# Kernel optimization log

Measured on AMD Instinct MI355X. Metric: run time of the kernel, lower is better.

Reference implementation:

```python
import jax, jax.numpy as jnp
import numpy as np

B, T, C = 1, 2048, 1024
H = 16
HD = C // H
BLOCK = 2048
NEG = float('-inf')

def setup_inputs() -> dict:
    key = jax.random.key(0)
    ks = jax.random.split(key, 6)
    x = jax.random.normal(ks[0], (B, T, C), dtype=jnp.float32)
    cumulative_scores = jax.random.normal(ks[1], (B, T), dtype=jnp.float32) * 0.1
    padding_mask = jnp.ones((B, T), dtype=jnp.float32)
    token_index = jax.random.randint(ks[2], (B, T), 0, BLOCK).astype(jnp.int64)
    w_attn = jax.random.normal(ks[3], (C, 3 * C), dtype=jnp.float32) * (1.0 / np.sqrt(C))
    b_attn = jnp.zeros((3 * C,), dtype=jnp.float32)
    w_proj = jax.random.normal(ks[4], (C, C), dtype=jnp.float32) * (1.0 / np.sqrt(C))
    b_proj = jnp.zeros((C,), dtype=jnp.float32)
    return dict(x=x, cumulative_scores=cumulative_scores, padding_mask=padding_mask,
                token_index=token_index, w_attn=w_attn, b_attn=b_attn,
                w_proj=w_proj, b_proj=b_proj)

def _rotate_half(z):
    z1, z2 = z[..., : z.shape[-1] // 2], z[..., z.shape[-1] // 2 :]
    return jnp.concatenate((-z2, z1), axis=-1)

def reference(x, cumulative_scores, padding_mask, token_index, w_attn, b_attn, w_proj, b_proj):
    # fused QKV projection
    qkv = x @ w_attn + b_attn                      # (B,T,3C)
    q, k, v = jnp.split(qkv, 3, axis=2)
    q = q.reshape(B, T, H, HD).transpose(0, 2, 1, 3)  # (B,H,T,HD)
    k = k.reshape(B, T, H, HD).transpose(0, 2, 1, 3)
    v = v.reshape(B, T, H, HD).transpose(0, 2, 1, 3)

    # dynamic per-token RoPE positions: global token counts (original scatter
    # broadcasts indices over batch, so counts are global across all batches)
    cnt = jnp.zeros((BLOCK,), jnp.float32).at[token_index.reshape(-1)].add(1.0)
    per_tok = (1.0 / (cnt + 1e-10))[token_index]       # (B,T)
    partial = jnp.cumsum(per_tok, axis=-1)             # (B,T) fractional positions

    inv_freq = 1.0 / (10000.0 ** (jnp.arange(0, HD, 2, dtype=jnp.float32) / HD))
    freqs = partial[..., None] * inv_freq              # (B,T,HD/2)
    emb = jnp.concatenate((freqs, freqs), axis=-1)     # (B,T,HD)
    cos = jnp.cos(emb)[:, None]                        # (B,1,T,HD)
    sin = jnp.sin(emb)[:, None]
    q = q * cos + _rotate_half(q) * sin
    k = k * cos + _rotate_half(k) * sin

    # 'fork' plan: overwrite last channel
    q = q.at[..., -1].set(1.0)
    k = k.at[..., -1].set(jnp.broadcast_to(cumulative_scores[:, None, :], (B, H, T)))

    # additive causal + padding mask (B,T,T)
    causal = jnp.where(jnp.tril(jnp.ones((T, T), jnp.bool_)), 0.0, NEG)
    pm = jnp.take_along_axis(padding_mask, token_index, axis=1)     # (B,T)
    outer = pm[:, :, None] * pm[:, None, :]
    pad_add = jnp.where(outer.astype(jnp.bool_), 0.0, NEG)
    mask = causal[None, :, :] + pad_add                              # (B,T,T)

    # scale v by exp(cumulative_scores)
    v = v * jnp.exp(cumulative_scores)[:, None, :, None]

    scores = jnp.einsum('bhqd,bhkd->bhqk', q, k) / np.sqrt(HD) + mask[:, None]
    probs = jax.nn.softmax(scores, axis=-1)
    y = jnp.einsum('bhqk,bhkd->bhqd', probs, v)        # (B,H,T,HD)
    y = y.transpose(0, 2, 1, 3).reshape(B, T, C)
    return y @ w_proj + b_proj
```

## Files before the change

kernel.cpp:

```cpp
#include <hip/hip_runtime.h>
#include <math.h>

#define T 2048
#define C 1024
#define H 16
#define HD 64
#define N3 (3*C)
#define NBLOCK 2048

typedef __attribute__((ext_vector_type(8))) short bf16x8;
typedef __attribute__((ext_vector_type(4))) float f32x4;

#define MFMA16(a, b, c) __builtin_amdgcn_mfma_f32_16x16x32_bf16((a), (b), (c), 0, 0, 0)

__device__ inline short f2bf(float f) {
    unsigned u; __builtin_memcpy(&u, &f, 4);
    unsigned r = (u + 0x7fffu + ((u >> 16) & 1u)) >> 16;
    return (short)r;
}
__device__ inline float bf2f(short s) {
    unsigned u = ((unsigned)(unsigned short)s) << 16;
    float f; __builtin_memcpy(&f, &u, 4);
    return f;
}

__device__ inline void gload_lds16(const void* g, void* l) {
    __builtin_amdgcn_global_load_lds((const __attribute__((address_space(1))) unsigned int*)g,
                                     (__attribute__((address_space(3))) unsigned int*)l,
                                     16, 0, 0);
}

__global__ __launch_bounds__(256) void pre_kernel(const float* __restrict__ x,
                                                  const float* __restrict__ w_attn,
                                                  const float* __restrict__ w_proj,
                                                  const int* __restrict__ tok,
                                                  const float* __restrict__ padmask,
                                                  short* __restrict__ xb,
                                                  short* __restrict__ wabT,
                                                  short* __restrict__ wpbT,
                                                  float2* __restrict__ tab,
                                                  float* __restrict__ pm_tok) {
    int bid = blockIdx.x;
    int tid = threadIdx.x;
    if (bid == 3072) {
        __shared__ float cntS[NBLOCK];
        __shared__ float sums[256];
        #pragma unroll
        for (int j = 0; j < 8; ++j) cntS[tid * 8 + j] = 0.0f;
        __syncthreads();
        int tk[8];
        #pragma unroll
        for (int j = 0; j < 8; ++j) {
            tk[j] = tok[tid * 8 + j];
            atomicAdd(&cntS[tk[j]], 1.0f);
        }
        __syncthreads();
        float vals[8];
        float s = 0.0f;
        #pragma unroll
        for (int j = 0; j < 8; ++j) {
            s += 1.0f / (cntS[tk[j]] + 1e-10f);
            vals[j] = s;
            pm_tok[tid * 8 + j] = padmask[tk[j]];
        }
        sums[tid] = s;
        __syncthreads();
        for (int off = 1; off < 256; off <<= 1) {
            float v = (tid >= off) ? sums[tid - off] : 0.0f;
            __syncthreads();
            sums[tid] += v;
            __syncthreads();
        }
        float offset = (tid > 0) ? sums[tid - 1] : 0.0f;
        float invf[32];
        #pragma unroll
        for (int j = 0; j < 32; ++j)
            invf[j] = exp2f(-(float)j * (13.287712379549449f / 32.0f));
        #pragma unroll
        for (int e = 0; e < 8; ++e) {
            float p = offset + vals[e];
            float2* row = tab + (tid * 8 + e) * 32;
            #pragma unroll
            for (int j = 0; j < 32; ++j) {
                float s_, c_;
                __sincosf(p * invf[j], &s_, &c_);
                row[j] = make_float2(c_, s_);
            }
        }
        return;
    }
    if (bid < 2048) {
        int i = bid * 1024 + tid * 4;
        float4 v = *(const float4*)(x + i);
        short4 o;
        o.x = f2bf(v.x); o.y = f2bf(v.y); o.z = f2bf(v.z); o.w = f2bf(v.w);
        *(short4*)(xb + i) = o;
        return;
    }
    __shared__ float S[64][65];
    const float* in; short* out; int Kd, Nd, bx, by;
    if (bid < 2816) {
        int b = bid - 2048;
        bx = b % 48; by = b / 48;
        in = w_attn; out = wabT; Kd = C; Nd = N3;
    } else {
        int b = bid - 2816;
        bx = b % 16; by = b / 16;
        in = w_proj; out = wpbT; Kd = C; Nd = C;
    }
    int n0 = bx * 64, k0 = by * 64;
    #pragma unroll
    for (int i = 0; i < 16; ++i) {
        int lin = tid + i * 256;
        int r = lin >> 6, c = lin & 63;
        S[r][c] = in[(size_t)(k0 + r) * Nd + n0 + c];
    }
    __syncthreads();
    #pragma unroll
    for (int i = 0; i < 16; ++i) {
        int lin = tid + i * 256;
        int rn = lin >> 6, ck = lin & 63;
        out[(size_t)(n0 + rn) * Kd + k0 + ck] = f2bf(S[ck][rn]);
    }
}

template <int EPI>
__global__ __launch_bounds__(256) void gemm128x64(const short* __restrict__ A,
                                                  const short* __restrict__ Bt,
                                                  const float* __restrict__ bias,
                                                  void* __restrict__ Cout,
                                                  int N, int K,
                                                  const float2* __restrict__ tab,
                                                  const float* __restrict__ cumsc,
                                                  const float* __restrict__ pm_tok,
                                                  short* __restrict__ vbT) {
    __shared__ alignas(16) short As[2][128 * 64];
    __shared__ alignas(16) short Bs[2][64 * 64];
    int tid = threadIdx.x;
    int m0 = blockIdx.y * 128, n0 = blockIdx.x * 64;
    int w = tid >> 6, l = tid & 63;
    int lq = l & 15, g = l >> 4;
    int urow = l >> 3;
    int sw_col = ((l & 7) ^ urow) * 8;

    f32x4 acc[2][4] = {};

    auto stage = [&](int buf, int k0) {
        #pragma unroll
        for (int i = 0; i < 4; ++i) {
            int u = w * 4 + i;
            gload_lds16(A + (size_t)(m0 + u * 8 + urow) * K + k0 + sw_col, As[buf] + u * 512);
        }
        #pragma unroll
        for (int i = 0; i < 2; ++i) {
            int u = w * 2 + i;
            gload_lds16(Bt + (size_t)(n0 + u * 8 + urow) * K + k0 + sw_col, Bs[buf] + u * 512);
        }
    };

    int NK = K / 64;
    stage(0, 0);
    asm volatile("s_waitcnt vmcnt(0)" ::: "memory");
    __builtin_amdgcn_s_barrier();
    __builtin_amdgcn_sched_barrier(0);

    for (int t = 0; t < NK; ++t) {
        int cur = t & 1;
        if (t + 1 < NK) stage(cur ^ 1, (t + 1) * 64);
        #pragma unroll
        for (int kk = 0; kk < 2; ++kk) {
            bf16x8 af[2], bfr[4];
            #pragma unroll
            for (int fi = 0; fi < 2; ++fi) {
                int rd = w * 32 + fi * 16 + lq;
                af[fi] = *(const bf16x8*)(As[cur] + rd * 64 + (((kk * 4 + g) ^ (rd & 7)) * 8));
            }
            #pragma unroll
            for (int fj = 0; fj < 4; ++fj) {
                int rd = fj * 16 + lq;
                bfr[fj] = *(const bf16x8*)(Bs[cur] + rd * 64 + (((kk * 4 + g) ^ (rd & 7)) * 8));
            }
            __builtin_amdgcn_s_setprio(1);
            #pragma unroll
            for (int fi = 0; fi < 2; ++fi)
                #pragma unroll
                for (int fj = 0; fj < 4; ++fj)
                    acc[fi][fj] = MFMA16(af[fi], bfr[fj], acc[fi][fj]);
            __builtin_amdgcn_s_setprio(0);
        }
        asm volatile("s_waitcnt vmcnt(0)" ::: "memory");
        __builtin_amdgcn_s_barrier();
        __builtin_amdgcn_sched_barrier(0);
    }

    if (EPI == 0) {
        float* Cf = (float*)Cout;
        #pragma unroll
        for (int fi = 0; fi < 2; ++fi)
            #pragma unroll
            for (int r = 0; r < 4; ++r) {
                int m = m0 + w * 32 + fi * 16 + g * 4 + r;
                #pragma unroll
                for (int fj = 0; fj < 4; ++fj) {
                    int n = n0 + fj * 16 + lq;
                    Cf[(size_t)m * N + n] = acc[fi][fj][r] + bias[n];
                }
            }
    } else {
        short* Cb = (short*)Cout;
        int nt = n0 >> 6;
        if (nt < 32) {
            bool isQ = (nt < 16);
            #pragma unroll
            for (int fi = 0; fi < 2; ++fi)
                #pragma unroll
                for (int r = 0; r < 4; ++r) {
                    int trow = m0 + w * 32 + fi * 16 + g * 4 + r;
                    float pm = pm_tok[trow];
                    float csc = cumsc[trow];
                    float2 cs0 = tab[trow * 32 + lq];
                    float2 cs1 = tab[trow * 32 + 16 + lq];
                    float a0 = acc[fi][0][r] + bias[n0 + lq];
                    float a1 = acc[fi][1][r] + bias[n0 + 16 + lq];
                    float a2 = acc[fi][2][r] + bias[n0 + 32 + lq];
                    float a3 = acc[fi][3][r] + bias[n0 + 48 + lq];
                    float lo0 = a0 * cs0.x - a2 * cs0.y;
                    float hi0 = a2 * cs0.x + a0 * cs0.y;
                    float lo1 = a1 * cs1.x - a3 * cs1.y;
                    float hi1 = a3 * cs1.x + a1 * cs1.y;
                    if (lq == 15)
                        hi1 = isQ ? ((pm != 0.0f) ? 1.0f : 0.0f)
                                  : ((pm != 0.0f) ? csc : -1e20f);
                    size_t base = (size_t)trow * N3 + n0;
                    Cb[base + lq]      = f2bf(lo0);
                    Cb[base + 16 + lq] = f2bf(lo1);
                    Cb[base + 32 + lq] = f2bf(hi0);
                    Cb[base + 48 + lq] = f2bf(hi1);
                }
        } else {
            int h = nt - 32;
            short* Sv = &As[0][0];
            __syncthreads();
            #pragma unroll
            for (int fi = 0; fi < 2; ++fi)
                #pragma unroll
                for (int r = 0; r < 4; ++r) {
                    int tloc = w * 32 + fi * 16 + g * 4 + r;
                    float ef = __expf(cumsc[m0 + tloc]);
                    #pragma unroll
                    for (int fj = 0; fj < 4; ++fj) {
                        int d = fj * 16 + lq;
                        Sv[d * 136 + tloc] = f2bf((acc[fi][fj][r] + bias[n0 + d]) * ef);
                    }
                }
            __syncthreads();
            #pragma unroll
            for (int e = 0; e < 4; ++e) {
                int idx = tid * 4 + e;
                int d = idx >> 4, t8 = (idx & 15) * 8;
                bf16x8 o = *(const bf16x8*)(Sv + d * 136 + t8);
                *(bf16x8*)(vbT + (size_t)(h * 64 + d) * T + m0 + t8) = o;
            }
        }
    }
}

__global__ __launch_bounds__(256) void attn_flash(const short* __restrict__ qkvb,
                                                  const short* __restrict__ vbT,
                                                  short* __restrict__ yb) {
    __shared__ alignas(16) short Kt[2][64 * 64];
    __shared__ alignas(16) short Vt[2][64 * 64];
    __shared__ alignas(16) short Ps[4][16][72];

    int b = blockIdx.x;
    int h, qt;
    if (b < 256) { h = b & 15; qt = 31 - (b >> 4); }
    else         { int c2 = b - 256; h = c2 & 15; qt = c2 >> 4; }
    int tid = threadIdx.x;
    int w = tid >> 6, l = tid & 63;
    int lq = l & 15, g = l >> 4;
    int qrl = w * 16 + lq;

    const short* qbase = qkvb + (size_t)(qt * 64 + qrl) * N3 + h * 64;
    bf16x8 qf0 = *(const bf16x8*)(qbase + g * 8);
    bf16x8 qf1 = *(const bf16x8*)(qbase + 32 + g * 8);

    f32x4 accO[4] = {};
    float lsum = 0.0f;

    int srow = tid >> 3, scol = (tid & 7) * 8;
    const short* kgb = qkvb + C + h * 64 + scol;
    const short* vgb = vbT + (size_t)(h * 64) * T + scol;
    int wb0 = srow * 128 + ((scol * 2) ^ ((srow & 7) << 4));
    int wb1 = (srow + 32) * 128 + ((scol * 2) ^ ((srow & 7) << 4));

    auto do_tile = [&](int cur, bool masked) {
        const char* Kc = (const char*)Kt[cur];
        const char* Vc = (const char*)Vt[cur];
        f32x4 s[4] = {};
        __builtin_amdgcn_s_setprio(1);
        #pragma unroll
        for (int f = 0; f < 4; ++f) {
            int row = f * 16 + lq;
            const char* kr_ = Kc + row * 128;
            int sw = (row & 7) << 4;
            bf16x8 a0 = *(const bf16x8*)(kr_ + ((g * 16) ^ sw));
            bf16x8 a1 = *(const bf16x8*)(kr_ + ((64 + g * 16) ^ sw));
            s[f] = MFMA16(a0, qf0, s[f]);
            s[f] = MFMA16(a1, qf1, s[f]);
        }
        __builtin_amdgcn_s_setprio(0);
        float p[16];
        #pragma unroll
        for (int f = 0; f < 4; ++f)
            #pragma unroll
            for (int r = 0; r < 4; ++r) {
                float sv = s[f][r] * 0.125f;
                if (masked) {
                    int kl = f * 16 + g * 4 + r;
                    sv = (kl > qrl) ? -INFINITY : sv;
                }
                float pv = __expf(sv);
                p[f * 4 + r] = pv;
                lsum += pv;
            }
        #pragma unroll
        for (int f = 0; f < 4; ++f) {
            unsigned u0, u1;
            asm("v_cvt_pk_bf16_f32 %0, %1, %2" : "=v"(u0) : "v"(p[f * 4 + 0]), "v"(p[f * 4 + 1]));
            asm("v_cvt_pk_bf16_f32 %0, %1, %2" : "=v"(u1) : "v"(p[f * 4 + 2]), "v"(p[f * 4 + 3]));
            uint2 uu; uu.x = u0; uu.y = u1;
            *(uint2*)&Ps[w][lq][f * 16 + g * 4] = uu;
        }
        __builtin_amdgcn_s_setprio(1);
        #pragma unroll
        for (int kh = 0; kh < 2; ++kh) {
            bf16x8 pa = *(const bf16x8*)&Ps[w][lq][kh * 32 + g * 8];
            #pragma unroll
            for (int f = 0; f < 4; ++f) {
                int vrow = f * 16 + lq;
                const char* vr_ = Vc + vrow * 128;
                bf16x8 vb = *(const bf16x8*)(vr_ + (((kh * 32 + g * 8) * 2) ^ ((vrow & 7) << 4)));
                accO[f] = MFMA16(pa, vb, accO[f]);
            }
        }
        __builtin_amdgcn_s_setprio(0);
    };

    uint4 kr0 = *(const uint4*)(kgb + (size_t)srow * N3);
    uint4 kr1 = *(const uint4*)(kgb + (size_t)(srow + 32) * N3);
    uint4 vr0 = *(const uint4*)(vgb + (size_t)srow * T);
    uint4 vr1 = *(const uint4*)(vgb + (size_t)(srow + 32) * T);
    *(uint4*)((char*)Kt[0] + wb0) = kr0;
    *(uint4*)((char*)Kt[0] + wb1) = kr1;
    *(uint4*)((char*)Vt[0] + wb0) = vr0;
    *(uint4*)((char*)Vt[0] + wb1) = vr1;
    __syncthreads();

    for (int t = 0; t < qt; ++t) {
        int kn = (t + 1) * 64;
        kr0 = *(const uint4*)(kgb + (size_t)(kn + srow) * N3);
        kr1 = *(const uint4*)(kgb + (size_t)(kn + srow + 32) * N3);
        vr0 = *(const uint4*)(vgb + (size_t)srow * T + kn);
        vr1 = *(const uint4*)(vgb + (size_t)(srow + 32) * T + kn);

        do_tile(t & 1, false);

        int nxt = (t & 1) ^ 1;
        *(uint4*)((char*)Kt[nxt] + wb0) = kr0;
        *(uint4*)((char*)Kt[nxt] + wb1) = kr1;
        *(uint4*)((char*)Vt[nxt] + wb0) = vr0;
        *(uint4*)((char*)Vt[nxt] + wb1) = vr1;
        __syncthreads();
    }
    do_tile(qt & 1, true);

    lsum += __shfl_xor(lsum, 16);
    lsum += __shfl_xor(lsum, 32);
    float linv_own = 1.0f / lsum;
    float li[4];
    #pragma unroll
    for (int r = 0; r < 4; ++r) li[r] = __shfl(linv_own, g * 4 + r);

    #pragma unroll
    for (int f = 0; f < 4; ++f)
        #pragma unroll
        for (int r = 0; r < 4; ++r) {
            int trow = qt * 64 + w * 16 + g * 4 + r;
            yb[(size_t)trow * C + h * 64 + f * 16 + lq] = f2bf(accO[f][r] * li[r]);
        }
}

extern "C" void kernel_launch(void* const* d_in, const int* in_sizes, int n_in,
                              void* d_out, int out_size, void* d_ws, size_t ws_size,
                              hipStream_t stream) {
    const float* x       = (const float*)d_in[0];
    const float* cumsc   = (const float*)d_in[1];
    const float* padmask = (const float*)d_in[2];
    const int*   tok     = (const int*)d_in[3];
    const float* w_attn  = (const float*)d_in[4];
    const float* b_attn  = (const float*)d_in[5];
    const float* w_proj  = (const float*)d_in[6];
    const float* b_proj  = (const float*)d_in[7];
    float* out = (float*)d_out;

    float*  pm_tok = (float*)d_ws;
    float2* tab    = (float2*)(pm_tok + 2048);
    short*  xb     = (short*)(pm_tok + 2048 + 131072);
    short*  wabT   = xb + (size_t)T * C;
    short*  wpbT   = wabT + (size_t)N3 * C;
    short*  qkvb   = wpbT + (size_t)C * C;
    short*  vbT    = qkvb + (size_t)T * N3;
    short*  yb     = vbT + (size_t)C * T;

    pre_kernel<<<3073, 256, 0, stream>>>(x, w_attn, w_proj, tok, padmask,
                                         xb, wabT, wpbT, tab, pm_tok);
    gemm128x64<1><<<dim3(48, 16), 256, 0, stream>>>(xb, wabT, b_attn, qkvb, N3, C,
                                                    tab, cumsc, pm_tok, vbT);
    attn_flash<<<512, 256, 0, stream>>>(qkvb, vbT, yb);
    gemm128x64<0><<<dim3(16, 16), 256, 0, stream>>>(yb, wpbT, b_proj, out, C, C,
                                                    nullptr, nullptr, nullptr, nullptr);
}
```

Measured before the change: 94.67 us.

## Retile GEMMs to 128xBN with BK=32 and 2x2 warp grid, direct V-transpose stores

```diff
diff --git a/kernel.cpp b/kernel.cpp
--- a/kernel.cpp
+++ b/kernel.cpp
@@ -124,41 +124,43 @@
     }
 }
 
-template <int EPI>
-__global__ __launch_bounds__(256) void gemm128x64(const short* __restrict__ A,
-                                                  const short* __restrict__ Bt,
-                                                  const float* __restrict__ bias,
-                                                  void* __restrict__ Cout,
-                                                  int N, int K,
-                                                  const float2* __restrict__ tab,
-                                                  const float* __restrict__ cumsc,
-                                                  const float* __restrict__ pm_tok,
-                                                  short* __restrict__ vbT) {
-    __shared__ alignas(16) short As[2][128 * 64];
-    __shared__ alignas(16) short Bs[2][64 * 64];
+template <int OUT_BF16, int BNF, int EPI>
+__global__ __launch_bounds__(256) void gemm_bt(const short* __restrict__ A,
+                                               const short* __restrict__ Bt,
+                                               const float* __restrict__ bias,
+                                               void* __restrict__ Cout,
+                                               int M, int N, int K,
+                                               const float2* __restrict__ tab,
+                                               const float* __restrict__ cumsc,
+                                               const float* __restrict__ pm_tok,
+                                               short* __restrict__ vbT) {
+    constexpr int BN = BNF * 32;
+    __shared__ alignas(16) short As[2][128 * 32];
+    __shared__ alignas(16) short Bs[2][BN * 32];
     int tid = threadIdx.x;
-    int m0 = blockIdx.y * 128, n0 = blockIdx.x * 64;
+    int m0 = blockIdx.y * 128, n0 = blockIdx.x * BN;
     int w = tid >> 6, l = tid & 63;
+    int wm = (w >> 1) * 64, wn = (w & 1) * (BNF * 16);
     int lq = l & 15, g = l >> 4;
-    int urow = l >> 3;
-    int sw_col = ((l & 7) ^ urow) * 8;
-
-    f32x4 acc[2][4] = {};
+    int prow = l >> 2, pcol = (l & 3) * 8;
+    f32x4 acc[4][BNF] = {};
 
     auto stage = [&](int buf, int k0) {
         #pragma unroll
-        for (int i = 0; i < 4; ++i) {
-            int u = w * 4 + i;
-            gload_lds16(A + (size_t)(m0 + u * 8 + urow) * K + k0 + sw_col, As[buf] + u * 512);
-        }
-        #pragma unroll
         for (int i = 0; i < 2; ++i) {
-            int u = w * 2 + i;
-            gload_lds16(Bt + (size_t)(n0 + u * 8 + urow) * K + k0 + sw_col, Bs[buf] + u * 512);
+            int c = w * 2 + i;
+            int row = c * 16 + prow;
+            gload_lds16(A + (size_t)(m0 + row) * K + k0 + pcol, As[buf] + c * 512);
+        }
+        #pragma unroll
+        for (int i = 0; i < BNF / 2; ++i) {
+            int c = w * (BNF / 2) + i;
+            int row = c * 16 + prow;
+            gload_lds16(Bt + (size_t)(n0 + row) * K + k0 + pcol, Bs[buf] + c * 512);
         }
     };
 
-    int NK = K / 64;
+    int NK = K / 32;
     stage(0, 0);
     asm volatile("s_waitcnt vmcnt(0)" ::: "memory");
     __builtin_amdgcn_s_barrier();
@@ -166,64 +168,62 @@
 
     for (int t = 0; t < NK; ++t) {
         int cur = t & 1;
-        if (t + 1 < NK) stage(cur ^ 1, (t + 1) * 64);
-        #pragma unroll
-        for (int kk = 0; kk < 2; ++kk) {
-            bf16x8 af[2], bfr[4];
-            #pragma unroll
-            for (int fi = 0; fi < 2; ++fi) {
-                int rd = w * 32 + fi * 16 + lq;
-                af[fi] = *(const bf16x8*)(As[cur] + rd * 64 + (((kk * 4 + g) ^ (rd & 7)) * 8));
-            }
-            #pragma unroll
-            for (int fj = 0; fj < 4; ++fj) {
-                int rd = fj * 16 + lq;
-                bfr[fj] = *(const bf16x8*)(Bs[cur] + rd * 64 + (((kk * 4 + g) ^ (rd & 7)) * 8));
-            }
-            __builtin_amdgcn_s_setprio(1);
-            #pragma unroll
-            for (int fi = 0; fi < 2; ++fi)
-                #pragma unroll
-                for (int fj = 0; fj < 4; ++fj)
-                    acc[fi][fj] = MFMA16(af[fi], bfr[fj], acc[fi][fj]);
-            __builtin_amdgcn_s_setprio(0);
-        }
+        if (t + 1 < NK) stage(cur ^ 1, (t + 1) * 32);
+
+        bf16x8 af[4], bfr[BNF];
+        #pragma unroll
+        for (int f = 0; f < 4; ++f)
+            af[f] = *(const bf16x8*)(As[cur] + (wm + f * 16 + lq) * 32 + g * 8);
+        #pragma unroll
+        for (int j = 0; j < BNF; ++j)
+            bfr[j] = *(const bf16x8*)(Bs[cur] + (wn + j * 16 + lq) * 32 + g * 8);
+        __builtin_amdgcn_s_setprio(1);
+        #pragma unroll
+        for (int fi = 0; fi < 4; ++fi)
+            #pragma unroll
+            for (int fj = 0; fj < BNF; ++fj)
+                acc[fi][fj] = MFMA16(af[fi], bfr[fj], acc[fi][fj]);
+        __builtin_amdgcn_s_setprio(0);
+
         asm volatile("s_waitcnt vmcnt(0)" ::: "memory");
         __builtin_amdgcn_s_barrier();
         __builtin_amdgcn_sched_barrier(0);
     }
 
     if (EPI == 0) {
-        float* Cf = (float*)Cout;
-        #pragma unroll
-        for (int fi = 0; fi < 2; ++fi)
-            #pragma unroll
-            for (int r = 0; r < 4; ++r) {
-                int m = m0 + w * 32 + fi * 16 + g * 4 + r;
+        #pragma unroll
+        for (int fi = 0; fi < 4; ++fi)
+            #pragma unroll
+            for (int fj = 0; fj < BNF; ++fj)
                 #pragma unroll
-                for (int fj = 0; fj < 4; ++fj) {
-                    int n = n0 + fj * 16 + lq;
-                    Cf[(size_t)m * N + n] = acc[fi][fj][r] + bias[n];
+                for (int r = 0; r < 4; ++r) {
+                    int m = m0 + wm + fi * 16 + g * 4 + r;
+                    int n = n0 + wn + fj * 16 + lq;
+                    float v = acc[fi][fj][r] + bias[n];
+                    if (OUT_BF16) ((short*)Cout)[(size_t)m * N + n] = f2bf(v);
+                    else          ((float*)Cout)[(size_t)m * N + n] = v;
                 }
-            }
     } else {
         short* Cb = (short*)Cout;
-        int nt = n0 >> 6;
-        if (nt < 32) {
-            bool isQ = (nt < 16);
-            #pragma unroll
-            for (int fi = 0; fi < 2; ++fi)
+        int section = n0 >> 10;
+        int cb = n0 + wn;
+        float b0 = bias[cb + lq],      b1 = bias[cb + 16 + lq];
+        float b2 = bias[cb + 32 + lq], b3 = bias[cb + 48 + lq];
+        if (section < 2) {
+            bool isQ = (section == 0);
+            #pragma unroll
+            for (int fi = 0; fi < 4; ++fi)
                 #pragma unroll
                 for (int r = 0; r < 4; ++r) {
-                    int trow = m0 + w * 32 + fi * 16 + g * 4 + r;
+                    int trow = m0 + wm + fi * 16 + g * 4 + r;
                     float pm = pm_tok[trow];
                     float csc = cumsc[trow];
                     float2 cs0 = tab[trow * 32 + lq];
                     float2 cs1 = tab[trow * 32 + 16 + lq];
-                    float a0 = acc[fi][0][r] + bias[n0 + lq];
-                    float a1 = acc[fi][1][r] + bias[n0 + 16 + lq];
-                    float a2 = acc[fi][2][r] + bias[n0 + 32 + lq];
-                    float a3 = acc[fi][3][r] + bias[n0 + 48 + lq];
+                    float a0 = acc[fi][0][r] + b0;
+                    float a1 = acc[fi][1][r] + b1;
+                    float a2 = acc[fi][2][r] + b2;
+                    float a3 = acc[fi][3][r] + b3;
                     float lo0 = a0 * cs0.x - a2 * cs0.y;
                     float hi0 = a2 * cs0.x + a0 * cs0.y;
                     float lo1 = a1 * cs1.x - a3 * cs1.y;
@@ -231,35 +231,31 @@
                     if (lq == 15)
                         hi1 = isQ ? ((pm != 0.0f) ? 1.0f : 0.0f)
                                   : ((pm != 0.0f) ? csc : -1e20f);
-                    size_t base = (size_t)trow * N3 + n0;
+                    size_t base = (size_t)trow * N3 + cb;
                     Cb[base + lq]      = f2bf(lo0);
                     Cb[base + 16 + lq] = f2bf(lo1);
                     Cb[base + 32 + lq] = f2bf(hi0);
                     Cb[base + 48 + lq] = f2bf(hi1);
                 }
         } else {
-            int h = nt - 32;
-            short* Sv = &As[0][0];
-            __syncthreads();
-            #pragma unroll
-            for (int fi = 0; fi < 2; ++fi)
+            int h = (cb - 2 * C) >> 6;
+            #pragma unroll
+            for (int fi = 0; fi < 4; ++fi) {
+                int tb = m0 + wm + fi * 16 + g * 4;
+                float ef[4];
                 #pragma unroll
-                for (int r = 0; r < 4; ++r) {
-                    int tloc = w * 32 + fi * 16 + g * 4 + r;
-                    float ef = __expf(cumsc[m0 + tloc]);
-                    #pragma unroll
-                    for (int fj = 0; fj < 4; ++fj) {
-                        int d = fj * 16 + lq;
-                        Sv[d * 136 + tloc] = f2bf((acc[fi][fj][r] + bias[n0 + d]) * ef);
-                    }
+                for (int r = 0; r < 4; ++r) ef[r] = __expf(cumsc[tb + r]);
+                #pragma unroll
+                for (int fj = 0; fj < 4; ++fj) {
+                    int d = fj * 16 + lq;
+                    float bv = bias[cb + fj * 16 + lq];
+                    short4 o;
+                    o.x = f2bf((acc[fi][fj][0] + bv) * ef[0]);
+                    o.y = f2bf((acc[fi][fj][1] + bv) * ef[1]);
+                    o.z = f2bf((acc[fi][fj][2] + bv) * ef[2]);
+                    o.w = f2bf((acc[fi][fj][3] + bv) * ef[3]);
+                    *(short4*)(vbT + (size_t)(h * 64 + d) * T + tb) = o;
                 }
-            __syncthreads();
-            #pragma unroll
-            for (int e = 0; e < 4; ++e) {
-                int idx = tid * 4 + e;
-                int d = idx >> 4, t8 = (idx & 15) * 8;
-                bf16x8 o = *(const bf16x8*)(Sv + d * 136 + t8);
-                *(bf16x8*)(vbT + (size_t)(h * 64 + d) * T + m0 + t8) = o;
             }
         }
     }
@@ -415,9 +411,9 @@
 
     pre_kernel<<<3073, 256, 0, stream>>>(x, w_attn, w_proj, tok, padmask,
                                          xb, wabT, wpbT, tab, pm_tok);
-    gemm128x64<1><<<dim3(48, 16), 256, 0, stream>>>(xb, wabT, b_attn, qkvb, N3, C,
-                                                    tab, cumsc, pm_tok, vbT);
+    gemm_bt<1, 4, 1><<<dim3(N3 / 128, T / 128), 256, 0, stream>>>(
+        xb, wabT, b_attn, qkvb, T, N3, C, tab, cumsc, pm_tok, vbT);
     attn_flash<<<512, 256, 0, stream>>>(qkvb, vbT, yb);
-    gemm128x64<0><<<dim3(16, 16), 256, 0, stream>>>(yb, wpbT, b_proj, out, C, C,
-                                                    nullptr, nullptr, nullptr, nullptr);
-}
+    gemm_bt<0, 2, 0><<<dim3(C / 64, T / 128), 256, 0, stream>>>(
+        yb, wpbT, b_proj, out, T, C, C, nullptr, nullptr, nullptr, nullptr);
+}
```

Measured after the change: 104.4 us. 10.3% more time.
